# Performance work log

Hardware: AMD Instinct MI355X
Metric: run time of the kernel (lower is better)

The kernel has to match this reference:

```python
import jax, jax.numpy as jnp
import numpy as np

D_MODEL = 2048
D_INNER = 2048
D_XB = 1024
D_STATE = 128          # SSM state size == attention head_dim
NHEADS = D_INNER // D_STATE   # 16
NKV = D_XB // D_STATE         # 8 kv-style heads for x (V) and B (K)
NREP = NHEADS // NKV          # 2 (GQA repeat)
D_CONV = 4
CHUNK = 128
INTER = 8192
EPS = 1e-5
BATCH, SEQ = 2, 2048


def setup_inputs() -> dict:
    key = jax.random.key(0)
    ks = jax.random.split(key, 8)
    conv_dim = 2 * D_XB + D_INNER            # conv over concat(x, B, C)
    proj_dim = 2 * D_INNER + 2 * D_XB + NHEADS  # z, x, B, C, dt
    g = lambda k, shape, sc: jax.random.normal(k, shape, jnp.float32) * sc
    return {
        "hidden_states": jax.random.normal(ks[0], (BATCH, SEQ, D_MODEL), jnp.float32),
        "ln1_w": jnp.ones((D_MODEL,), jnp.float32),
        "W_in": g(ks[1], (D_MODEL, proj_dim), 0.02),
        "conv_w": g(ks[2], (D_CONV, conv_dim), 0.2),
        "conv_b": jnp.zeros((conv_dim,), jnp.float32),
        "dt_bias": jnp.log(jnp.expm1(jnp.linspace(1e-3, 0.1, NHEADS))).astype(jnp.float32),
        "A_log": jnp.log(jnp.linspace(1.0, 16.0, NHEADS)).astype(jnp.float32),
        "D": jnp.ones((NHEADS,), jnp.float32),
        "norm_w": jnp.ones((D_INNER,), jnp.float32),
        "W_out": g(ks[3], (D_INNER, D_MODEL), 0.02),
        "ln2_w": jnp.ones((D_MODEL,), jnp.float32),
        "w1": g(ks[4], (D_MODEL, INTER), 0.02),
        "w3": g(ks[5], (D_MODEL, INTER), 0.02),
        "w2": g(ks[6], (INTER, D_MODEL), 0.02),
    }


def _rmsnorm(x, w, eps=EPS):
    v = jnp.mean(x * x, axis=-1, keepdims=True)
    return x * jax.lax.rsqrt(v + eps) * w


def _segsum(x):
    # x: (..., T) -> lower-triangular pairwise cumulative sums (..., T, T)
    T = x.shape[-1]
    cs = jnp.cumsum(x, axis=-1)
    seg = cs[..., :, None] - cs[..., None, :]
    mask = jnp.tril(jnp.ones((T, T), bool))
    return jnp.where(mask, seg, -jnp.inf)


def _ssd(X, dA, Bm, Cm, chunk):
    # Chunked SSD (Mamba2). X:(b,l,h,p) already dt-weighted, dA:(b,l,h), Bm/Cm:(b,l,h,n)
    b, l, h, p = X.shape
    c = l // chunk
    X = X.reshape(b, c, chunk, h, p)
    Bm = Bm.reshape(b, c, chunk, h, -1)
    Cm = Cm.reshape(b, c, chunk, h, -1)
    dA = dA.reshape(b, c, chunk, h).transpose(0, 3, 1, 2)  # (b,h,c,l)
    dA_cs = jnp.cumsum(dA, axis=-1)
    L = jnp.exp(_segsum(dA))  # (b,h,c,l,l) causal decay matrix
    Y_diag = jnp.einsum("bclhn,bcshn,bhcls,bcshp->bclhp", Cm, Bm, L, X)
    decay_states = jnp.exp(dA_cs[..., -1:] - dA_cs)  # (b,h,c,l)
    states = jnp.einsum("bcshn,bhcs,bcshp->bchpn", Bm, decay_states, X)
    states = jnp.concatenate([jnp.zeros_like(states[:, :1]), states], axis=1)
    chunk_decay = jnp.exp(_segsum(jnp.pad(dA_cs[..., -1], ((0, 0), (0, 0), (1, 0)))))  # (b,h,c+1,c+1)
    new_states = jnp.einsum("bhzc,bchpn->bzhpn", chunk_decay, states)
    prev_states = new_states[:, :-1]  # state entering each chunk
    Y_off = jnp.einsum("bclhn,bchpn,bhcl->bclhp", Cm, prev_states, jnp.exp(dA_cs))
    return (Y_diag + Y_off).reshape(b, l, h, p)


def reference(hidden_states, ln1_w, W_in, conv_w, conv_b, dt_bias, A_log, D,
              norm_w, W_out, ln2_w, w1, w3, w2):
    b, l, _ = hidden_states.shape
    # --- Mamba2 mixer branch ---
    res = hidden_states
    h = _rmsnorm(hidden_states, ln1_w)
    zxbcdt = h @ W_in
    splits = np.cumsum([D_INNER, D_XB, D_XB, D_INNER]).tolist()
    z, xv, Bv, Cv, dt = jnp.split(zxbcdt, splits, axis=-1)
    # causal depthwise conv over concat(x,B,C), then SiLU
    xBC = jnp.concatenate([xv, Bv, Cv], axis=-1)
    xp = jnp.pad(xBC, ((0, 0), (D_CONV - 1, 0), (0, 0)))
    conv = sum(xp[:, k:k + l, :] * conv_w[k] for k in range(D_CONV)) + conv_b
    xBC = jax.nn.silu(conv)
    xv, Bv, Cv = jnp.split(xBC, [D_XB, 2 * D_XB], axis=-1)
    # GQA-style head layout: x,B have NKV heads repeated to NHEADS; C has NHEADS
    xh = jnp.repeat(xv.reshape(b, l, NKV, D_STATE), NREP, axis=2)  # (b,l,H,P)
    Bh = jnp.repeat(Bv.reshape(b, l, NKV, D_STATE), NREP, axis=2)  # (b,l,H,N)
    Ch = Cv.reshape(b, l, NHEADS, D_STATE)                         # (b,l,H,N)
    dt = jax.nn.softplus(dt + dt_bias)       # (b,l,H)
    a = -jnp.exp(A_log)                      # (H,) negative decay rates
    dA = dt * a                              # (b,l,H) log-decay
    X = xh * dt[..., None]
    y = _ssd(X, dA, Bh, Ch, CHUNK)
    y = y + D[None, None, :, None] * xh      # skip connection
    y = y.reshape(b, l, D_INNER)
    y = _rmsnorm(y * jax.nn.silu(z), norm_w)  # gated RMSNorm
    h = y @ W_out
    h = res + h
    # --- SwiGLU MLP branch ---
    res2 = h
    h = _rmsnorm(h, ln2_w)
    h = (jax.nn.silu(h @ w1) * (h @ w3)) @ w2
    return res2 + h
```

## Files before the change

kernel.cpp:

```cpp
#include <hip/hip_runtime.h>
#include <hip/hip_bf16.h>

typedef __hip_bfloat16 bf16;
typedef __attribute__((ext_vector_type(8))) short short8_t;
typedef __attribute__((ext_vector_type(4))) short short4_t;
typedef __attribute__((ext_vector_type(4))) float floatx4;

#define T_ 4096

__device__ __forceinline__ float b2f(bf16 v) { return __bfloat162float(v); }
__device__ __forceinline__ bf16 f2b(float v) { return __float2bfloat16(v); }
__device__ __forceinline__ float siluf(float v) { return v / (1.f + expf(-v)); }

#define ASYNC_CP16(g, l) __builtin_amdgcn_global_load_lds( \
    (const __attribute__((address_space(1))) unsigned int*)(g), \
    (__attribute__((address_space(3))) unsigned int*)(l), 16, 0, 0)

__device__ __forceinline__ void ld8f(const bf16* p, float* f) {
  union { short8_t v; bf16 h[8]; } u;
  u.v = *(const short8_t*)p;
#pragma unroll
  for (int e = 0; e < 8; e++) f[e] = b2f(u.h[e]);
}
__device__ __forceinline__ void st8f(bf16* p, const float* f) {
  union { short8_t v; bf16 h[8]; } u;
#pragma unroll
  for (int e = 0; e < 8; e++) u.h[e] = f2b(f[e]);
  *(short8_t*)p = u.v;
}
__device__ __forceinline__ void cp8(bf16* d, const bf16* s) {
  *(short8_t*)d = *(const short8_t*)s;
}
__device__ __forceinline__ void ld4f(const bf16* p, float* f) {
  union { short4_t v; bf16 h[4]; } u;
  u.v = *(const short4_t*)p;
#pragma unroll
  for (int e = 0; e < 4; e++) f[e] = b2f(u.h[e]);
}
__device__ __forceinline__ float ldw1(const void* p, size_t i, int isbf) {
  return isbf ? b2f(((const bf16*)p)[i]) : ((const float*)p)[i];
}
__device__ __forceinline__ void ld8w(const void* p, size_t base, int isbf, float* f) {
  if (isbf) { ld8f((const bf16*)p + base, f); }
  else {
    const float4 a = *(const float4*)((const float*)p + base);
    const float4 b4 = *(const float4*)((const float*)p + base + 4);
    f[0] = a.x; f[1] = a.y; f[2] = a.z; f[3] = a.w;
    f[4] = b4.x; f[5] = b4.y; f[6] = b4.z; f[7] = b4.w;
  }
}
__device__ __forceinline__ void ld4w(const void* p, size_t base, int isbf, float* f) {
  if (isbf) { ld4f((const bf16*)p + base, f); }
  else {
    const float4 a = *(const float4*)((const float*)p + base);
    f[0] = a.x; f[1] = a.y; f[2] = a.z; f[3] = a.w;
  }
}

__global__ void detect_kernel(const unsigned int* __restrict__ ln1w, int* __restrict__ flag)
{
  if (threadIdx.x == 0) flag[0] = (ln1w[0] == 0x3F803F80u) ? 1 : 0;
}

__global__ __launch_bounds__(256)
void wtrans_kernel(const void* __restrict__ src, bf16* __restrict__ dst,
                   int K, int N, const int* __restrict__ flag)
{
  const int isbf = *flag;
  __shared__ bf16 tile[64][65];
  const int n0 = blockIdx.x * 64, k0 = blockIdx.y * 64;
  const int tid = threadIdx.x;
  const int kk = tid >> 4;
  const int nn = (tid & 15) * 4;
#pragma unroll
  for (int r = 0; r < 64; r += 16) {
    const int k = k0 + kk + r;
    float v[4];
    if (n0 + nn < N) ld4w(src, (size_t)k * N + n0 + nn, isbf, v);
    else { v[0] = v[1] = v[2] = v[3] = 0.f; }
#pragma unroll
    for (int e = 0; e < 4; e++) tile[kk + r][nn + e] = f2b(v[e]);
  }
  __syncthreads();
  const int nw = tid >> 4;
  const int kw = (tid & 15) * 4;
#pragma unroll
  for (int r = 0; r < 64; r += 16) {
    union { short4_t v; bf16 h[4]; } u;
#pragma unroll
    for (int e = 0; e < 4; e++) u.h[e] = tile[kw + e][nw + r];
    *(short4_t*)(dst + (size_t)(n0 + nw + r) * K + k0 + kw) = u.v;
  }
}

__global__ __launch_bounds__(256)
void rms_kernel(const void* __restrict__ x, int xstride, int xmode,
                const bf16* __restrict__ z, int zstride,
                const void* __restrict__ w, const int* __restrict__ flag,
                bf16* __restrict__ out)
{
  const int isbf = *flag;
  const int xb = xmode ? 1 : isbf;
  const int t = blockIdx.x;
  const int base = threadIdx.x * 8;
  float u[8];
  ld8w(x, (size_t)t * xstride + base, xb, u);
  if (z) {
    float zv[8];
    ld8f(z + (size_t)t * zstride + base, zv);
#pragma unroll
    for (int i = 0; i < 8; i++) u[i] *= siluf(zv[i]);
  }
  float s = 0.f;
#pragma unroll
  for (int i = 0; i < 8; i++) s += u[i] * u[i];
#pragma unroll
  for (int o = 32; o > 0; o >>= 1) s += __shfl_down(s, o, 64);
  __shared__ float red[4];
  if ((threadIdx.x & 63) == 0) red[threadIdx.x >> 6] = s;
  __syncthreads();
  const float tot = red[0] + red[1] + red[2] + red[3];
  const float sc = rsqrtf(tot * (1.f / 2048.f) + 1e-5f);
  float wv[8];
  ld8w(w, base, isbf, wv);
#pragma unroll
  for (int i = 0; i < 8; i++) u[i] = u[i] * sc * wv[i];
  st8f(out + (size_t)t * 2048 + base, u);
}

template <int BN, int RESMODE, int OUTMODE>
__global__ __launch_bounds__(512, 2)
void gemm256(const bf16* __restrict__ A, const bf16* __restrict__ Bt,
             const void* __restrict__ RES, void* __restrict__ C,
             int M, int N, int K, const int* __restrict__ flag)
{
  constexpr int NF = BN / 64;
  constexpr int WCOL = BN / 4;
  __shared__ bf16 As[4][256][32];
  __shared__ bf16 Bs[4][BN][32];

  const int isbf = (RESMODE == 2 || OUTMODE == 1) ? *flag : 0;
  const int tid  = threadIdx.x;
  const int lane = tid & 63;
  const int wave = tid >> 6;
  const int wr = wave >> 2;
  const int wc = wave & 3;
  const int lo = lane & 15, quad = lane >> 4;
  const int m0 = blockIdx.y * 256, n0 = blockIdx.x * BN;

  const int lr = lane >> 2;
  const int lc = (lane & 3) * 8;

  auto stageA = [&](int t2, int j) {
    bf16* ld = &As[t2 & 3][wave * 32 + j * 16][0];
    const bf16* g = A + (size_t)(m0 + wave * 32 + j * 16 + lr) * K + t2 * 32 + lc;
    ASYNC_CP16(g, ld);
  };
  auto stageB = [&](int t2, int j) {
    const int r0 = (BN == 256) ? (wave * 32 + j * 16) : (wave * 16);
    bf16* ld = &Bs[t2 & 3][r0][0];
    const bf16* g = Bt + (size_t)(n0 + r0 + lr) * K + t2 * 32 + lc;
    ASYNC_CP16(g, ld);
  };
  auto wait_lpt = []() {
    if constexpr (BN == 256) asm volatile("s_waitcnt vmcnt(4)" ::: "memory");
    else                     asm volatile("s_waitcnt vmcnt(3)" ::: "memory");
  };

  const int NT = K >> 5;
  floatx4 acc[8][NF] = {};

  stageA(0, 0); stageB(0, 0); stageA(0, 1); if constexpr (BN == 256) stageB(0, 1);
  stageA(1, 0); stageB(1, 0); stageA(1, 1); if constexpr (BN == 256) stageB(1, 1);
  wait_lpt();
  __builtin_amdgcn_s_barrier();
  __builtin_amdgcn_sched_barrier(0);

#pragma unroll 1
  for (int t = 0; t < NT; ++t) {
    const int slot = t & 3;
    const bool pf = (t + 2 < NT);
    const bf16* as = &As[slot][0][0];
    const bf16* bs = &Bs[slot][0][0];

    short8_t bfv[NF];
#pragma unroll
    for (int nf = 0; nf < NF; nf++)
      bfv[nf] = *(const short8_t*)(bs + (wc * WCOL + nf * 16 + lo) * 32 + quad * 8);

    short8_t af[4];
#pragma unroll
    for (int mf = 0; mf < 4; mf++)
      af[mf] = *(const short8_t*)(as + (wr * 128 + mf * 16 + lo) * 32 + quad * 8);
    if (pf) { stageA(t + 2, 0); stageB(t + 2, 0); }
    __builtin_amdgcn_s_setprio(1);
#pragma unroll
    for (int mf = 0; mf < 4; mf++)
#pragma unroll
      for (int nf = 0; nf < NF; nf++)
        acc[mf][nf] = __builtin_amdgcn_mfma_f32_16x16x32_bf16(af[mf], bfv[nf], acc[mf][nf], 0, 0, 0);
    __builtin_amdgcn_s_setprio(0);

#pragma unroll
    for (int mf = 0; mf < 4; mf++)
      af[mf] = *(const short8_t*)(as + (wr * 128 + 64 + mf * 16 + lo) * 32 + quad * 8);
    if (pf) { stageA(t + 2, 1); if constexpr (BN == 256) stageB(t + 2, 1); }
    __builtin_amdgcn_s_setprio(1);
#pragma unroll
    for (int mf = 0; mf < 4; mf++)
#pragma unroll
      for (int nf = 0; nf < NF; nf++)
        acc[4 + mf][nf] = __builtin_amdgcn_mfma_f32_16x16x32_bf16(af[mf], bfv[nf], acc[4 + mf][nf], 0, 0, 0);
    __builtin_amdgcn_s_setprio(0);

    __builtin_amdgcn_sched_barrier(0);
    if (pf) wait_lpt();
    else    asm volatile("s_waitcnt vmcnt(0)" ::: "memory");
    __builtin_amdgcn_s_barrier();
    __builtin_amdgcn_sched_barrier(0);
  }

#pragma unroll
  for (int mt = 0; mt < 8; mt++)
#pragma unroll
    for (int nf = 0; nf < NF; nf++) {
      const int col = n0 + wc * WCOL + nf * 16 + lo;
      if (col < N) {
#pragma unroll
        for (int r = 0; r < 4; r++) {
          const int row = m0 + wr * 128 + mt * 16 + quad * 4 + r;
          float v = acc[mt][nf][r];
          const size_t idx = (size_t)row * N + col;
          if (RESMODE == 1) v += b2f(((const bf16*)RES)[idx]);
          if (RESMODE == 2) v += isbf ? b2f(((const bf16*)RES)[idx]) : ((const float*)RES)[idx];
          if (RESMODE == 3) v = siluf(v) * b2f(((const bf16*)RES)[idx]);
          if (OUTMODE == 0) ((bf16*)C)[idx] = f2b(v);
          else {
            if (isbf) ((bf16*)C)[idx] = f2b(v);
            else      ((float*)C)[idx] = v;
          }
        }
      }
    }
}

__global__ __launch_bounds__(256)
void conv_kernel(const bf16* __restrict__ zx, const void* __restrict__ cw,
                 const void* __restrict__ cb, const int* __restrict__ flag,
                 bf16* __restrict__ xbc)
{
  const int isbf = *flag;
  const int t = blockIdx.y;
  const int b = t >> 11, l = t & 2047;
  const int c = blockIdx.x * 1024 + threadIdx.x * 4;
  float acc[4];
  ld4w(cb, c, isbf, acc);
#pragma unroll
  for (int k = 0; k < 4; k++) {
    const int tl = l + k - 3;
    if (tl >= 0) {
      float xv[4], wv[4];
      ld4f(zx + (size_t)(b * 2048 + tl) * 6160 + 2048 + c, xv);
      ld4w(cw, (size_t)k * 4096 + c, isbf, wv);
#pragma unroll
      for (int j = 0; j < 4; j++) acc[j] += xv[j] * wv[j];
    }
  }
  union { short4_t v; bf16 h[4]; } u;
#pragma unroll
  for (int j = 0; j < 4; j++) u.h[j] = f2b(siluf(acc[j]));
  *(short4_t*)(xbc + (size_t)t * 4096 + c) = u.v;
}

__global__ void dt_kernel(const bf16* __restrict__ zx, const void* __restrict__ dt_bias,
                          const void* __restrict__ A_log, const int* __restrict__ flag,
                          float* __restrict__ dtb, float* __restrict__ dAcs,
                          float* __restrict__ dAsum)
{
  const int isbf = *flag;
  const int b = blockIdx.x;
  const int h = threadIdx.x & 15, c = threadIdx.x >> 4;
  const float bias = ldw1(dt_bias, h, isbf);
  const float a = -expf(ldw1(A_log, h, isbf));
  float cum = 0.f;
  for (int s = 0; s < 128; s++) {
    const int t = b * 2048 + c * 128 + s;
    float dtv = b2f(zx[(size_t)t * 6160 + 6144 + h]) + bias;
    dtv = (dtv > 20.f) ? dtv : log1pf(expf(dtv));
    cum += dtv * a;
    dtb[(size_t)t * 16 + h] = dtv;
    dAcs[(size_t)t * 16 + h] = cum;
  }
  dAsum[(b * 16 + c) * 16 + h] = cum;
}

__global__ __launch_bounds__(256)
void ssd_states(const bf16* __restrict__ xbc, const float* __restrict__ dtb,
                const float* __restrict__ dAcs, const float* __restrict__ dAsum,
                float* __restrict__ states)
{
  const int blk = blockIdx.x;
  const int h = blk & 15, c = (blk >> 4) & 15, b = blk >> 8;
  const int kv = h >> 1;
  const int tid = threadIdx.x;
  __shared__ bf16 Bt[128 * 128];
  __shared__ bf16 Xs[128 * 128];
  const float dAs = dAsum[(b * 16 + c) * 16 + h];
  for (int i = 0; i < 8; i++) {
    const int idx = (i * 256 + tid) * 8;
    const int s = idx >> 7, j = idx & 127;
    const size_t trow = (size_t)(b * 2048 + c * 128 + s);
    cp8(&Bt[idx], xbc + trow * 4096 + 1024 + kv * 128 + j);
    float xv[8];
    ld8f(xbc + trow * 4096 + kv * 128 + j, xv);
    const float sc = dtb[trow * 16 + h] * expf(dAs - dAcs[trow * 16 + h]);
#pragma unroll
    for (int e = 0; e < 8; e++) xv[e] *= sc;
    st8f(&Xs[idx], xv);
  }
  __syncthreads();
  const int pt = (tid >> 4) * 8, nt = (tid & 15) * 8;
  float acc[8][8] = {};
  for (int s = 0; s < 128; s++) {
    float xr[8], br[8];
    ld8f(&Xs[s * 128 + pt], xr);
    ld8f(&Bt[s * 128 + nt], br);
#pragma unroll
    for (int i = 0; i < 8; i++)
#pragma unroll
      for (int j = 0; j < 8; j++) acc[i][j] += xr[i] * br[j];
  }
  float* sp = states + (size_t)blk * 16384;
#pragma unroll
  for (int i = 0; i < 8; i++)
#pragma unroll
    for (int j4 = 0; j4 < 8; j4 += 4) {
      floatx4 v;
#pragma unroll
      for (int e = 0; e < 4; e++) v[e] = acc[i][j4 + e];
      *(floatx4*)&sp[(pt + i) * 128 + nt + j4] = v;
    }
}

__global__ __launch_bounds__(256)
void ssd_scan(const float* __restrict__ dAsum, float* __restrict__ states)
{
  const int b = blockIdx.x >> 4, h = blockIdx.x & 15;
  const int tid = threadIdx.x;
  float run[64];
#pragma unroll
  for (int i = 0; i < 64; i++) run[i] = 0.f;
  for (int c = 0; c < 16; c++) {
    const float dec = expf(dAsum[(b * 16 + c) * 16 + h]);
    float* sp = states + ((size_t)((b * 16 + c) * 16 + h)) * 16384;
    for (int i = 0; i < 64; i++) {
      const int k = tid + 256 * i;
      const float v = sp[k];
      sp[k] = run[i];
      run[i] = run[i] * dec + v;
    }
  }
}

__global__ __launch_bounds__(256)
void ssd_s(const bf16* __restrict__ xbc, const float* __restrict__ dAcs,
           bf16* __restrict__ Sbuf)
{
  const int blk = blockIdx.x;
  const int h = blk & 15, c = (blk >> 4) & 15, b = blk >> 8;
  const int kv = h >> 1;
  const int tid = threadIdx.x;
  __shared__ bf16 Ct[128 * 128];
  __shared__ bf16 Bt[128 * 128];
  for (int i = 0; i < 8; i++) {
    const int idx = (i * 256 + tid) * 8;
    const int s = idx >> 7, j = idx & 127;
    const size_t trow = (size_t)(b * 2048 + c * 128 + s);
    cp8(&Ct[idx], xbc + trow * 4096 + 2048 + h * 128 + j);
    cp8(&Bt[idx], xbc + trow * 4096 + 1024 + kv * 128 + j);
  }
  __syncthreads();
  const int lt = (tid >> 4) * 8, st = (tid & 15) * 8;
  float sv[8][8] = {};
  for (int nn = 0; nn < 128; nn += 8) {
    float cf[8][8];
#pragma unroll
    for (int i = 0; i < 8; i++) ld8f(&Ct[(lt + i) * 128 + nn], cf[i]);
#pragma unroll
    for (int j = 0; j < 8; j++) {
      float bv[8];
      ld8f(&Bt[(st + j) * 128 + nn], bv);
#pragma unroll
      for (int i = 0; i < 8; i++) {
        float d = 0.f;
#pragma unroll
        for (int e = 0; e < 8; e++) d += cf[i][e] * bv[e];
        sv[i][j] += d;
      }
    }
  }
  const int tb = b * 2048 + c * 128;
  float la[8], sa[8];
#pragma unroll
  for (int i = 0; i < 8; i++) la[i] = dAcs[(size_t)(tb + lt + i) * 16 + h];
#pragma unroll
  for (int j = 0; j < 8; j++) sa[j] = dAcs[(size_t)(tb + st + j) * 16 + h];
  bf16* so = Sbuf + (size_t)blk * 16384;
#pragma unroll
  for (int i = 0; i < 8; i++) {
    float o[8];
#pragma unroll
    for (int j = 0; j < 8; j++) {
      const int l = lt + i, s2 = st + j;
      o[j] = (l >= s2) ? sv[i][j] * expf(la[i] - sa[j]) : 0.f;
    }
    st8f(&so[(lt + i) * 128 + st], o);
  }
}

__global__ __launch_bounds__(256)
void ssd_y(const bf16* __restrict__ xbc, const float* __restrict__ dtb,
           const float* __restrict__ dAcs, const float* __restrict__ prev,
           const bf16* __restrict__ Sbuf, const void* __restrict__ Dp,
           const int* __restrict__ flag, bf16* __restrict__ y)
{
  const int isbf = *flag;
  const int blk = blockIdx.x;
  const int h = blk & 15, c = (blk >> 4) & 15, b = blk >> 8;
  const int kv = h >> 1;
  const int tid = threadIdx.x;
  __shared__ bf16 L1[128 * 128];
  __shared__ bf16 L2[128 * 128];
  for (int i = 0; i < 8; i++) {
    const int idx = (i * 256 + tid) * 8;
    const int s = idx >> 7, j = idx & 127;
    const size_t trow = (size_t)(b * 2048 + c * 128 + s);
    cp8(&L1[idx], Sbuf + (size_t)blk * 16384 + idx);
    float xv[8];
    ld8f(xbc + trow * 4096 + kv * 128 + j, xv);
    const float dt = dtb[trow * 16 + h];
#pragma unroll
    for (int e = 0; e < 8; e++) xv[e] *= dt;
    st8f(&L2[idx], xv);
  }
  __syncthreads();
  const int lt = (tid >> 4) * 8, pt = (tid & 15) * 8;
  float acc[8][8] = {};
  for (int s8 = 0; s8 < 128; s8 += 8) {
    float sf[8][8];
#pragma unroll
    for (int i = 0; i < 8; i++) ld8f(&L1[(lt + i) * 128 + s8], sf[i]);
#pragma unroll
    for (int e = 0; e < 8; e++) {
      float xr[8];
      ld8f(&L2[(s8 + e) * 128 + pt], xr);
#pragma unroll
      for (int i = 0; i < 8; i++)
#pragma unroll
        for (int j = 0; j < 8; j++) acc[i][j] += sf[i][e] * xr[j];
    }
  }
  __syncthreads();
  for (int i = 0; i < 8; i++) {
    const int idx = (i * 256 + tid) * 8;
    const int s = idx >> 7, j = idx & 127;
    const size_t trow = (size_t)(b * 2048 + c * 128 + s);
    cp8(&L1[idx], xbc + trow * 4096 + 2048 + h * 128 + j);
  }
  for (int i = 0; i < 16; i++) {
    const int idx = (i * 256 + tid) * 4;
    const int p = idx >> 7, n = idx & 127;
    floatx4 pv = *(const floatx4*)(prev + (size_t)blk * 16384 + idx);
#pragma unroll
    for (int e = 0; e < 4; e++) L2[(n + e) * 128 + p] = f2b(pv[e]);
  }
  __syncthreads();
  const int tb = b * 2048 + c * 128;
  float er[8];
#pragma unroll
  for (int i = 0; i < 8; i++) er[i] = expf(dAcs[(size_t)(tb + lt + i) * 16 + h]);
  for (int n8 = 0; n8 < 128; n8 += 8) {
    float cf[8][8];
#pragma unroll
    for (int i = 0; i < 8; i++) {
      ld8f(&L1[(lt + i) * 128 + n8], cf[i]);
#pragma unroll
      for (int e = 0; e < 8; e++) cf[i][e] *= er[i];
    }
#pragma unroll
    for (int e = 0; e < 8; e++) {
      float pv8[8];
      ld8f(&L2[(n8 + e) * 128 + pt], pv8);
#pragma unroll
      for (int i = 0; i < 8; i++)
#pragma unroll
        for (int j = 0; j < 8; j++) acc[i][j] += cf[i][e] * pv8[j];
    }
  }
  const float Dh = ldw1(Dp, h, isbf);
#pragma unroll
  for (int i = 0; i < 8; i++) {
    const size_t trow = (size_t)(tb + lt + i);
    float xv[8];
    ld8f(xbc + trow * 4096 + kv * 128 + pt, xv);
    float o[8];
#pragma unroll
    for (int j = 0; j < 8; j++) o[j] = acc[i][j] + Dh * xv[j];
    st8f(y + trow * 2048 + h * 128 + pt, o);
  }
}

extern "C" void kernel_launch(void* const* d_in, const int* in_sizes, int n_in,
                              void* d_out, int out_size, void* d_ws, size_t ws_size,
                              hipStream_t stream)
{
  const void* hs      = d_in[0];
  const void* ln1_w   = d_in[1];
  const void* W_in    = d_in[2];
  const void* conv_w  = d_in[3];
  const void* conv_b  = d_in[4];
  const void* dt_bias = d_in[5];
  const void* A_log   = d_in[6];
  const void* Dp      = d_in[7];
  const void* norm_w  = d_in[8];
  const void* W_out   = d_in[9];
  const void* ln2_w   = d_in[10];
  const void* w1      = d_in[11];
  const void* w3      = d_in[12];
  const void* w2      = d_in[13];
  char* ws = (char*)d_ws;

  size_t off = 0;
  auto take = [&](size_t bytes) {
    char* p = ws + off;
    off += (bytes + 255) & ~(size_t)255;
    return p;
  };
  int*   flag   = (int*)take(256);
  bf16*  h_norm = (bf16*)take((size_t)T_ * 2048 * 2);
  bf16*  zx     = (bf16*)take((size_t)T_ * 6160 * 2);
  bf16*  xbc    = (bf16*)take((size_t)T_ * 4096 * 2);
  float* dtb    = (float*)take((size_t)T_ * 16 * 4);
  float* dacs   = (float*)take((size_t)T_ * 16 * 4);
  float* dasum  = (float*)take(2 * 16 * 16 * 4);
  float* states = (float*)take((size_t)512 * 16384 * 4);
  bf16*  Sbuf   = (bf16*)take((size_t)512 * 16384 * 2);
  bf16*  ybuf   = (bf16*)take((size_t)T_ * 2048 * 2);
  bf16*  res2   = (bf16*)take((size_t)T_ * 2048 * 2);
  bf16*  Wt_in  = (bf16*)take((size_t)6400 * 2048 * 2);
  bf16*  Wt_out = (bf16*)take((size_t)2048 * 2048 * 2);
  bf16*  tbuf = zx;
  bf16*  w1t  = (bf16*)states;
  bf16*  w3t  = Sbuf;
  bf16*  w2t  = Wt_in;

  detect_kernel<<<1, 64, 0, stream>>>((const unsigned int*)ln1_w, flag);
  wtrans_kernel<<<dim3(100, 32), 256, 0, stream>>>(W_in, Wt_in, 2048, 6160, flag);
  wtrans_kernel<<<dim3(32, 32), 256, 0, stream>>>(W_out, Wt_out, 2048, 2048, flag);
  rms_kernel<<<T_, 256, 0, stream>>>(hs, 2048, 0, nullptr, 0, ln1_w, flag, h_norm);
  gemm256<256, 0, 0><<<dim3(25, 16), 512, 0, stream>>>(h_norm, Wt_in, nullptr, zx, 4096, 6160, 2048, flag);
  conv_kernel<<<dim3(4, T_), 256, 0, stream>>>(zx, conv_w, conv_b, flag, xbc);
  dt_kernel<<<2, 256, 0, stream>>>(zx, dt_bias, A_log, flag, dtb, dacs, dasum);
  ssd_states<<<512, 256, 0, stream>>>(xbc, dtb, dacs, dasum, states);
  ssd_scan<<<32, 256, 0, stream>>>(dasum, states);
  ssd_s<<<512, 256, 0, stream>>>(xbc, dacs, Sbuf);
  ssd_y<<<512, 256, 0, stream>>>(xbc, dtb, dacs, states, Sbuf, Dp, flag, ybuf);
  rms_kernel<<<T_, 256, 0, stream>>>(ybuf, 2048, 1, zx, 6160, norm_w, flag, h_norm);
  gemm256<128, 2, 0><<<dim3(16, 16), 512, 0, stream>>>(h_norm, Wt_out, hs, res2, 4096, 2048, 2048, flag);
  wtrans_kernel<<<dim3(128, 32), 256, 0, stream>>>(w1, w1t, 2048, 8192, flag);
  wtrans_kernel<<<dim3(128, 32), 256, 0, stream>>>(w3, w3t, 2048, 8192, flag);
  wtrans_kernel<<<dim3(32, 128), 256, 0, stream>>>(w2, w2t, 8192, 2048, flag);
  rms_kernel<<<T_, 256, 0, stream>>>(res2, 2048, 1, nullptr, 0, ln2_w, flag, h_norm);
  gemm256<256, 0, 0><<<dim3(32, 16), 512, 0, stream>>>(h_norm, w3t, nullptr, tbuf, 4096, 8192, 2048, flag);
  gemm256<256, 3, 0><<<dim3(32, 16), 512, 0, stream>>>(h_norm, w1t, tbuf, tbuf, 4096, 8192, 2048, flag);
  gemm256<128, 1, 1><<<dim3(16, 16), 512, 0, stream>>>(tbuf, w2t, res2, d_out, 4096, 2048, 8192, flag);
}
```

Measured before the change: 1.401 ms.

## Rework GEMM to BK=64 swizzled double-buffer, add split-K for N=2048 GEMMs

```diff
diff --git a/kernel.cpp b/kernel.cpp
--- a/kernel.cpp
+++ b/kernel.cpp
@@ -15,6 +15,8 @@
 #define ASYNC_CP16(g, l) __builtin_amdgcn_global_load_lds( \
     (const __attribute__((address_space(1))) unsigned int*)(g), \
     (__attribute__((address_space(3))) unsigned int*)(l), 16, 0, 0)
+
+#define VMCNT(n) asm volatile("s_waitcnt vmcnt(" #n ")" ::: "memory")
 
 __device__ __forceinline__ void ld8f(const bf16* p, float* f) {
   union { short8_t v; bf16 h[8]; } u;
@@ -128,120 +130,170 @@
   st8f(out + (size_t)t * 2048 + base, u);
 }
 
-template <int BN, int RESMODE, int OUTMODE>
+template <int RESMODE, int OUTMODE, int SPLITK>
 __global__ __launch_bounds__(512, 2)
 void gemm256(const bf16* __restrict__ A, const bf16* __restrict__ Bt,
              const void* __restrict__ RES, void* __restrict__ C,
              int M, int N, int K, const int* __restrict__ flag)
 {
-  constexpr int NF = BN / 64;
-  constexpr int WCOL = BN / 4;
-  __shared__ bf16 As[4][256][32];
-  __shared__ bf16 Bs[4][BN][32];
-
-  const int isbf = (RESMODE == 2 || OUTMODE == 1) ? *flag : 0;
+  __shared__ bf16 As[2][256][64];
+  __shared__ bf16 Bs[2][256][64];
+
+  const int isbf = (RESMODE == 2) ? *flag : 0;
   const int tid  = threadIdx.x;
   const int lane = tid & 63;
   const int wave = tid >> 6;
   const int wr = wave >> 2;
   const int wc = wave & 3;
   const int lo = lane & 15, quad = lane >> 4;
-  const int m0 = blockIdx.y * 256, n0 = blockIdx.x * BN;
-
-  const int lr = lane >> 2;
-  const int lc = (lane & 3) * 8;
-
-  auto stageA = [&](int t2, int j) {
-    bf16* ld = &As[t2 & 3][wave * 32 + j * 16][0];
-    const bf16* g = A + (size_t)(m0 + wave * 32 + j * 16 + lr) * K + t2 * 32 + lc;
+  const int m0 = blockIdx.y * 256, n0 = blockIdx.x * 256;
+  const int klen = K / SPLITK;
+  const int kbase = (SPLITK > 1) ? (int)blockIdx.z * klen : 0;
+  const int NT = klen >> 6;
+
+  const int srow = tid >> 3;
+  const int gsl  = (tid & 7) ^ (srow & 7);
+  auto stA = [&](int sl, int kk, int lbase) {
+    bf16* ld = &As[sl][lbase + (wave << 3)][0];
+    const bf16* g = A + (size_t)(m0 + lbase + srow) * K + kk + gsl * 8;
     ASYNC_CP16(g, ld);
   };
-  auto stageB = [&](int t2, int j) {
-    const int r0 = (BN == 256) ? (wave * 32 + j * 16) : (wave * 16);
-    bf16* ld = &Bs[t2 & 3][r0][0];
-    const bf16* g = Bt + (size_t)(n0 + r0 + lr) * K + t2 * 32 + lc;
+  auto stB = [&](int sl, int kk, int lbase, int add32) {
+    bf16* ld = &Bs[sl][lbase + (wave << 3)][0];
+    const int rr = (lbase + srow) & 127;
+    const int grow = (rr >> 5) * 64 + add32 + (rr & 31);
+    const bf16* g = Bt + (size_t)(n0 + grow) * K + kk + gsl * 8;
     ASYNC_CP16(g, ld);
   };
-  auto wait_lpt = []() {
-    if constexpr (BN == 256) asm volatile("s_waitcnt vmcnt(4)" ::: "memory");
-    else                     asm volatile("s_waitcnt vmcnt(3)" ::: "memory");
+
+  const int rsl0 = (0 * 4 + quad) ^ (lo & 7);
+  const int rsl1 = (1 * 4 + quad) ^ (lo & 7);
+  auto rdA = [&](const bf16* as, int mh, short8_t* dst) {
+#pragma unroll
+    for (int mf = 0; mf < 4; mf++) {
+      const int row = wr * 128 + mh * 64 + mf * 16 + lo;
+      dst[mf * 2 + 0] = *(const short8_t*)(as + row * 64 + rsl0 * 8);
+      dst[mf * 2 + 1] = *(const short8_t*)(as + row * 64 + rsl1 * 8);
+    }
   };
-
-  const int NT = K >> 5;
-  floatx4 acc[8][NF] = {};
-
-  stageA(0, 0); stageB(0, 0); stageA(0, 1); if constexpr (BN == 256) stageB(0, 1);
-  stageA(1, 0); stageB(1, 0); stageA(1, 1); if constexpr (BN == 256) stageB(1, 1);
-  wait_lpt();
-  __builtin_amdgcn_s_barrier();
-  __builtin_amdgcn_sched_barrier(0);
+  auto rdB = [&](const bf16* bs, int nh, short8_t* dst) {
+#pragma unroll
+    for (int nf = 0; nf < 2; nf++) {
+      const int rl = nh * 128 + wc * 32 + nf * 16 + lo;
+      dst[nf * 2 + 0] = *(const short8_t*)(bs + rl * 64 + rsl0 * 8);
+      dst[nf * 2 + 1] = *(const short8_t*)(bs + rl * 64 + rsl1 * 8);
+    }
+  };
+
+  floatx4 acc[8][4] = {};
+  short8_t af[8], b0f[4], b1f[4];
+
+#define MFMA_CLUSTER(MH, NH, BF)                                            \
+  __builtin_amdgcn_s_setprio(1);                                            \
+  _Pragma("unroll")                                                         \
+  for (int mf = 0; mf < 4; mf++)                                            \
+    _Pragma("unroll")                                                       \
+    for (int nf = 0; nf < 2; nf++)                                          \
+      _Pragma("unroll")                                                     \
+      for (int k = 0; k < 2; k++)                                           \
+        acc[(MH)*4 + mf][(NH)*2 + nf] = __builtin_amdgcn_mfma_f32_16x16x32_bf16( \
+            af[mf*2 + k], BF[nf*2 + k], acc[(MH)*4 + mf][(NH)*2 + nf], 0, 0, 0); \
+  __builtin_amdgcn_s_setprio(0);
+
+  {
+    const int kk = kbase;
+    stA(0, kk, 0);   stA(0, kk, 128);
+    stB(0, kk, 0, 0);   stB(0, kk, 64, 0);
+    stB(0, kk, 128, 32); stB(0, kk, 192, 32);
+    stA(0, kk, 64);  stA(0, kk, 192);
+  }
 
 #pragma unroll 1
   for (int t = 0; t < NT; ++t) {
-    const int slot = t & 3;
-    const bool pf = (t + 2 < NT);
-    const bf16* as = &As[slot][0][0];
-    const bf16* bs = &Bs[slot][0][0];
-
-    short8_t bfv[NF];
-#pragma unroll
-    for (int nf = 0; nf < NF; nf++)
-      bfv[nf] = *(const short8_t*)(bs + (wc * WCOL + nf * 16 + lo) * 32 + quad * 8);
-
-    short8_t af[4];
-#pragma unroll
-    for (int mf = 0; mf < 4; mf++)
-      af[mf] = *(const short8_t*)(as + (wr * 128 + mf * 16 + lo) * 32 + quad * 8);
-    if (pf) { stageA(t + 2, 0); stageB(t + 2, 0); }
-    __builtin_amdgcn_s_setprio(1);
-#pragma unroll
-    for (int mf = 0; mf < 4; mf++)
-#pragma unroll
-      for (int nf = 0; nf < NF; nf++)
-        acc[mf][nf] = __builtin_amdgcn_mfma_f32_16x16x32_bf16(af[mf], bfv[nf], acc[mf][nf], 0, 0, 0);
-    __builtin_amdgcn_s_setprio(0);
-
-#pragma unroll
-    for (int mf = 0; mf < 4; mf++)
-      af[mf] = *(const short8_t*)(as + (wr * 128 + 64 + mf * 16 + lo) * 32 + quad * 8);
-    if (pf) { stageA(t + 2, 1); if constexpr (BN == 256) stageB(t + 2, 1); }
-    __builtin_amdgcn_s_setprio(1);
-#pragma unroll
-    for (int mf = 0; mf < 4; mf++)
-#pragma unroll
-      for (int nf = 0; nf < NF; nf++)
-        acc[4 + mf][nf] = __builtin_amdgcn_mfma_f32_16x16x32_bf16(af[mf], bfv[nf], acc[4 + mf][nf], 0, 0, 0);
-    __builtin_amdgcn_s_setprio(0);
+    const int ct = t & 1, nt = ct ^ 1;
+    const bool pf = (t + 1 < NT);
+    const int kk = kbase + (t + 1) * 64;
+    const bf16* as = &As[ct][0][0];
+    const bf16* bs = &Bs[ct][0][0];
 
     __builtin_amdgcn_sched_barrier(0);
-    if (pf) wait_lpt();
-    else    asm volatile("s_waitcnt vmcnt(0)" ::: "memory");
+    VMCNT(4);
     __builtin_amdgcn_s_barrier();
     __builtin_amdgcn_sched_barrier(0);
-  }
-
-#pragma unroll
-  for (int mt = 0; mt < 8; mt++)
-#pragma unroll
-    for (int nf = 0; nf < NF; nf++) {
-      const int col = n0 + wc * WCOL + nf * 16 + lo;
+    rdA(as, 0, af);
+    rdB(bs, 0, b0f);
+    if (pf) { stA(nt, kk, 0); stA(nt, kk, 128); }
+    MFMA_CLUSTER(0, 0, b0f);
+
+    __builtin_amdgcn_sched_barrier(0);
+    if (pf) { VMCNT(4); } else { VMCNT(2); }
+    __builtin_amdgcn_s_barrier();
+    __builtin_amdgcn_sched_barrier(0);
+    rdB(bs, 1, b1f);
+    if (pf) { stB(nt, kk, 0, 0); stB(nt, kk, 64, 0); }
+    MFMA_CLUSTER(0, 1, b1f);
+
+    __builtin_amdgcn_sched_barrier(0);
+    if (pf) { VMCNT(4); } else { VMCNT(0); }
+    __builtin_amdgcn_s_barrier();
+    __builtin_amdgcn_sched_barrier(0);
+    rdA(as, 1, af);
+    if (pf) { stB(nt, kk, 128, 32); stB(nt, kk, 192, 32); }
+    MFMA_CLUSTER(1, 0, b0f);
+
+    if (pf) { stA(nt, kk, 64); stA(nt, kk, 192); }
+    MFMA_CLUSTER(1, 1, b1f);
+  }
+#undef MFMA_CLUSTER
+
+#pragma unroll
+  for (int mi = 0; mi < 8; mi++)
+#pragma unroll
+    for (int ni = 0; ni < 4; ni++) {
+      const int col = n0 + wc * 64 + ni * 16 + lo;
       if (col < N) {
 #pragma unroll
         for (int r = 0; r < 4; r++) {
-          const int row = m0 + wr * 128 + mt * 16 + quad * 4 + r;
-          float v = acc[mt][nf][r];
+          const int row = m0 + wr * 128 + mi * 16 + quad * 4 + r;
+          float v = acc[mi][ni][r];
           const size_t idx = (size_t)row * N + col;
           if (RESMODE == 1) v += b2f(((const bf16*)RES)[idx]);
           if (RESMODE == 2) v += isbf ? b2f(((const bf16*)RES)[idx]) : ((const float*)RES)[idx];
           if (RESMODE == 3) v = siluf(v) * b2f(((const bf16*)RES)[idx]);
           if (OUTMODE == 0) ((bf16*)C)[idx] = f2b(v);
-          else {
-            if (isbf) ((bf16*)C)[idx] = f2b(v);
-            else      ((float*)C)[idx] = v;
-          }
+          else ((float*)C)[(size_t)blockIdx.z * M * N + idx] = v;
         }
       }
     }
+}
+
+__global__ __launch_bounds__(256)
+void combine_kernel(const float* __restrict__ P, const void* __restrict__ RES,
+                    int resmode, void* __restrict__ OUT, int outext,
+                    const int* __restrict__ flag)
+{
+  const int isbf = *flag;
+  const size_t i = ((size_t)blockIdx.x * 256 + threadIdx.x) * 8;
+  const float* Q = P + (size_t)4096 * 2048;
+  float v[8], rv[8];
+#pragma unroll
+  for (int e = 0; e < 8; e += 4) {
+    const float4 a = *(const float4*)(P + i + e);
+    const float4 b4 = *(const float4*)(Q + i + e);
+    v[e + 0] = a.x + b4.x; v[e + 1] = a.y + b4.y;
+    v[e + 2] = a.z + b4.z; v[e + 3] = a.w + b4.w;
+  }
+  const int rbf = (resmode == 1) ? 1 : isbf;
+  ld8w(RES, i, rbf, rv);
+#pragma unroll
+  for (int e = 0; e < 8; e++) v[e] += rv[e];
+  if (outext && !isbf) {
+    float4 o0 = {v[0], v[1], v[2], v[3]}, o1 = {v[4], v[5], v[6], v[7]};
+    *(float4*)((float*)OUT + i) = o0;
+    *(float4*)((float*)OUT + i + 4) = o1;
+  } else {
+    st8f((bf16*)OUT + i, v);
+  }
 }
 
 __global__ __launch_bounds__(256)
@@ -346,19 +398,15 @@
 void ssd_scan(const float* __restrict__ dAsum, float* __restrict__ states)
 {
   const int b = blockIdx.x >> 4, h = blockIdx.x & 15;
-  const int tid = threadIdx.x;
-  float run[64];
-#pragma unroll
-  for (int i = 0; i < 64; i++) run[i] = 0.f;
+  const int base = blockIdx.y * 1024 + threadIdx.x * 4;
+  floatx4 run = {};
   for (int c = 0; c < 16; c++) {
     const float dec = expf(dAsum[(b * 16 + c) * 16 + h]);
-    float* sp = states + ((size_t)((b * 16 + c) * 16 + h)) * 16384;
-    for (int i = 0; i < 64; i++) {
-      const int k = tid + 256 * i;
-      const float v = sp[k];
-      sp[k] = run[i];
-      run[i] = run[i] * dec + v;
-    }
+    float* sp = states + ((size_t)((b * 16 + c) * 16 + h)) * 16384 + base;
+    floatx4 v = *(const floatx4*)sp;
+    *(floatx4*)sp = run;
+#pragma unroll
+    for (int e = 0; e < 4; e++) run[e] = run[e] * dec + v[e];
   }
 }
 
@@ -553,25 +601,28 @@
   bf16*  w1t  = (bf16*)states;
   bf16*  w3t  = Sbuf;
   bf16*  w2t  = Wt_in;
+  float* psplit = states;
 
   detect_kernel<<<1, 64, 0, stream>>>((const unsigned int*)ln1_w, flag);
   wtrans_kernel<<<dim3(100, 32), 256, 0, stream>>>(W_in, Wt_in, 2048, 6160, flag);
   wtrans_kernel<<<dim3(32, 32), 256, 0, stream>>>(W_out, Wt_out, 2048, 2048, flag);
   rms_kernel<<<T_, 256, 0, stream>>>(hs, 2048, 0, nullptr, 0, ln1_w, flag, h_norm);
-  gemm256<256, 0, 0><<<dim3(25, 16), 512, 0, stream>>>(h_norm, Wt_in, nullptr, zx, 4096, 6160, 2048, flag);
+  gemm256<0, 0, 1><<<dim3(25, 16), 512, 0, stream>>>(h_norm, Wt_in, nullptr, zx, 4096, 6160, 2048, flag);
   conv_kernel<<<dim3(4, T_), 256, 0, stream>>>(zx, conv_w, conv_b, flag, xbc);
   dt_kernel<<<2, 256, 0, stream>>>(zx, dt_bias, A_log, flag, dtb, dacs, dasum);
   ssd_states<<<512, 256, 0, stream>>>(xbc, dtb, dacs, dasum, states);
-  ssd_scan<<<32, 256, 0, stream>>>(dasum, states);
+  ssd_scan<<<dim3(32, 16), 256, 0, stream>>>(dasum, states);
   ssd_s<<<512, 256, 0, stream>>>(xbc, dacs, Sbuf);
   ssd_y<<<512, 256, 0, stream>>>(xbc, dtb, dacs, states, Sbuf, Dp, flag, ybuf);
   rms_kernel<<<T_, 256, 0, stream>>>(ybuf, 2048, 1, zx, 6160, norm_w, flag, h_norm);
-  gemm256<128, 2, 0><<<dim3(16, 16), 512, 0, stream>>>(h_norm, Wt_out, hs, res2, 4096, 2048, 2048, flag);
+  gemm256<0, 2, 2><<<dim3(8, 16, 2), 512, 0, stream>>>(h_norm, Wt_out, nullptr, psplit, 4096, 2048, 2048, flag);
+  combine_kernel<<<4096, 256, 0, stream>>>(psplit, hs, 2, res2, 0, flag);
   wtrans_kernel<<<dim3(128, 32), 256, 0, stream>>>(w1, w1t, 2048, 8192, flag);
   wtrans_kernel<<<dim3(128, 32), 256, 0, stream>>>(w3, w3t, 2048, 8192, flag);
   wtrans_kernel<<<dim3(32, 128), 256, 0, stream>>>(w2, w2t, 8192, 2048, flag);
   rms_kernel<<<T_, 256, 0, stream>>>(res2, 2048, 1, nullptr, 0, ln2_w, flag, h_norm);
-  gemm256<256, 0, 0><<<dim3(32, 16), 512, 0, stream>>>(h_norm, w3t, nullptr, tbuf, 4096, 8192, 2048, flag);
-  gemm256<256, 3, 0><<<dim3(32, 16), 512, 0, stream>>>(h_norm, w1t, tbuf, tbuf, 4096, 8192, 2048, flag);
-  gemm256<128, 1, 1><<<dim3(16, 16), 512, 0, stream>>>(tbuf, w2t, res2, d_out, 4096, 2048, 8192, flag);
-}
+  gemm256<0, 0, 1><<<dim3(32, 16), 512, 0, stream>>>(h_norm, w3t, nullptr, tbuf, 4096, 8192, 2048, flag);
+  gemm256<3, 0, 1><<<dim3(32, 16), 512, 0, stream>>>(h_norm, w1t, tbuf, tbuf, 4096, 8192, 2048, flag);
+  gemm256<0, 2, 2><<<dim3(8, 16, 2), 512, 0, stream>>>(tbuf, w2t, nullptr, psplit, 4096, 2048, 8192, flag);
+  combine_kernel<<<4096, 256, 0, stream>>>(psplit, res2, 1, d_out, 1, flag);
+}
```

After: 1.190 ms. 1.18x faster.
